# Optimization experiments

Measured on AMD Instinct MI355X. Metric: run time of the kernel, lower is better.

## Reference

```python
import jax, jax.numpy as jnp
import numpy as np
import math

INPUT_SIZE = 1024
HIDDEN_SIZE = 1024
BATCH = 4096


def setup_inputs() -> dict:
    key = jax.random.key(0)
    ks = jax.random.split(key, 16)
    stddev = 1.0 / math.sqrt(HIDDEN_SIZE)

    def unif(k, shape):
        return jax.random.uniform(k, shape, minval=-stddev, maxval=stddev, dtype=jnp.float32)

    inp = {
        'x': jax.random.normal(ks[0], (BATCH, INPUT_SIZE), dtype=jnp.float32),
        'h_prev': jax.random.normal(ks[1], (BATCH, HIDDEN_SIZE), dtype=jnp.float32),
        'c_prev': jax.random.normal(ks[2], (BATCH, HIDDEN_SIZE), dtype=jnp.float32),
        'igx': unif(ks[3], (INPUT_SIZE, HIDDEN_SIZE)),
        'igu': unif(ks[4], (HIDDEN_SIZE, HIDDEN_SIZE)),
        'ib': unif(ks[5], (HIDDEN_SIZE,)),
        'fgx': unif(ks[6], (INPUT_SIZE, HIDDEN_SIZE)),
        'fgu': unif(ks[7], (HIDDEN_SIZE, HIDDEN_SIZE)),
        'fb': unif(ks[8], (HIDDEN_SIZE,)),
        'ogx': unif(ks[9], (INPUT_SIZE, HIDDEN_SIZE)),
        'ogu': unif(ks[10], (HIDDEN_SIZE, HIDDEN_SIZE)),
        'ob': unif(ks[11], (HIDDEN_SIZE,)),
        'cgx': unif(ks[12], (INPUT_SIZE, HIDDEN_SIZE)),
        'cgu': unif(ks[13], (HIDDEN_SIZE, HIDDEN_SIZE)),
        'cb': unif(ks[14], (HIDDEN_SIZE,)),
    }
    return inp


def reference(x, h_prev, c_prev, igx, igu, ib, fgx, fgu, fb, ogx, ogu, ob, cgx, cgu, cb):
    # Fuse the 8 gate matmuls into 2 GEMMs via concatenated weights.
    # Wx: [input_size, 4H], Wh: [hidden, 4H], b: [4H]; gate order i,f,o,c.
    Wx = jnp.concatenate([igx, fgx, ogx, cgx], axis=1)
    Wh = jnp.concatenate([igu, fgu, ogu, cgu], axis=1)
    b = jnp.concatenate([ib, fb, ob, cb], axis=0)
    gates = x @ Wx + h_prev @ Wh + b  # [B, 4H]
    H = c_prev.shape[-1]
    ig = jax.nn.sigmoid(gates[:, 0 * H:1 * H])
    fg = jax.nn.sigmoid(gates[:, 1 * H:2 * H])
    og = jax.nn.sigmoid(gates[:, 2 * H:3 * H])
    cc = jnp.tanh(gates[:, 3 * H:4 * H])
    c = fg * c_prev + ig * cc
    h = og * jnp.tanh(c)
    return (h, c)
```

## Files before the change

### kernel.cpp

```cpp
#include <hip/hip_runtime.h>
#include <hip/hip_bf16.h>

typedef unsigned short u16;
typedef unsigned int u32;
typedef short bf16x8 __attribute__((ext_vector_type(8)));
typedef float f32x4 __attribute__((ext_vector_type(4)));
typedef u16 u16x8 __attribute__((ext_vector_type(8)));

#define HID 1024
#define BATCH 4096
#define KTOT 2048
#define NT 32
#define LDS_OP 16384

__device__ __forceinline__ u16 f2bf(float f) {
  u32 v = __builtin_bit_cast(u32, f);
  u32 r = (v + 0x7fffu + ((v >> 16) & 1u)) >> 16;
  return (u16)r;
}
__device__ __forceinline__ float sigmoid_fast(float x) {
  return 1.0f / (1.0f + __expf(-x));
}
__device__ __forceinline__ float tanh_fast(float x) {
  return 2.0f * sigmoid_fast(2.0f * x) - 1.0f;
}
__device__ __forceinline__ void gl_lds16(const void* g, void* l) {
  __builtin_amdgcn_global_load_lds(
      (const __attribute__((address_space(1))) u32*)g,
      (__attribute__((address_space(3))) u32*)l, 16, 0, 0);
}

__global__ __launch_bounds__(256) void prep_all(
    const float* __restrict__ x, const float* __restrict__ hp,
    const float* __restrict__ igx, const float* __restrict__ fgx,
    const float* __restrict__ ogx, const float* __restrict__ cgx,
    const float* __restrict__ igu, const float* __restrict__ fgu,
    const float* __restrict__ ogu, const float* __restrict__ cgu,
    u16* __restrict__ xh, u16* __restrict__ bt) {
  __shared__ u16 lds[64 * 66];
  if (blockIdx.x < 4096) {
    int c = blockIdx.x * 256 + threadIdx.x;
    int row = c >> 8;
    int col0 = (c & 255) << 3;
    const float* src = (col0 < 1024)
                           ? (x + (size_t)row * 1024 + col0)
                           : (hp + (size_t)row * 1024 + (col0 - 1024));
    f32x4 a = *(const f32x4*)(src);
    f32x4 b = *(const f32x4*)(src + 4);
    u16x8 v;
#pragma unroll
    for (int j = 0; j < 4; ++j) { v[j] = f2bf(a[j]); v[j + 4] = f2bf(b[j]); }
    *(u16x8*)(xh + (size_t)row * KTOT + col0) = v;
    return;
  }
  const float* srcs[8] = {igx, fgx, ogx, cgx, igu, fgu, ogu, cgu};
  int bid = blockIdx.x - 4096;
  int m = bid >> 8;
  int tile = bid & 255;
  int th = tile & 15, tk = tile >> 4;
  int h0 = th << 6, k0 = tk << 6;
  int g = m & 3, which = m >> 2;
  const float* W = srcs[m] + (size_t)k0 * HID + h0;

  int t = threadIdx.x;
  int r1 = t >> 4;
  int c1 = (t & 15) << 2;
#pragma unroll
  for (int p = 0; p < 4; ++p) {
    int row = (p << 4) + r1;
    f32x4 v = *(const f32x4*)(W + (size_t)row * HID + c1);
    u32 p0 = (u32)f2bf(v[0]) | ((u32)f2bf(v[1]) << 16);
    u32 p1 = (u32)f2bf(v[2]) | ((u32)f2bf(v[3]) << 16);
    u32* d = (u32*)&lds[row * 66 + c1];
    d[0] = p0;
    d[1] = p1;
  }
  __syncthreads();
  int nl = t >> 2;
  int kc = t & 3;
  int row_np = ((h0 >> 4) << 6) + ((nl >> 4) << 6) + (g << 4) + (nl & 15);
  size_t dst = (size_t)row_np * KTOT + (size_t)which * 1024 + k0;
  u16x8 a2, b2;
#pragma unroll
  for (int j = 0; j < 8; ++j) {
    a2[j] = lds[(kc * 8 + j) * 66 + nl];
    b2[j] = lds[(kc * 8 + 32 + j) * 66 + nl];
  }
  *(u16x8*)(&bt[dst + kc * 8]) = a2;
  *(u16x8*)(&bt[dst + kc * 8 + 32]) = b2;
}

__device__ __forceinline__ void stage(int s, const u16* aS, const u16* bS,
                                      u16* lds, int sx) {
  if (s >= 4 * NT) return;
  int ts = s >> 2, hh = s & 3;
  int op = (hh >> 1) ^ 1;
  int rb = (hh & 1) << 7;
  const u16* src = (op ? bS : aS) + (size_t)rb * KTOT + ts * 64;
  u16* dst = lds + ((((ts & 1) << 1) + op) * LDS_OP) + (rb << 6) + sx * 8;
  gl_lds16(src, dst);
  gl_lds16(src + (size_t)64 * KTOT, dst + 4096);
}

__global__ __launch_bounds__(512, 2) void lstm_gemm(
    const u16* __restrict__ xh, const u16* __restrict__ bt,
    const float* __restrict__ cprev,
    const float* __restrict__ ib, const float* __restrict__ fb,
    const float* __restrict__ ob, const float* __restrict__ cb,
    float* __restrict__ hout, float* __restrict__ cout) {
  __shared__ __align__(16) u16 lds[2 * 2 * LDS_OP];

  int sx = threadIdx.x;
  int bid = blockIdx.x;
  int xcd = bid & 7, lid = bid >> 3;
  int brow = ((xcd & 3) << 2) | (lid & 3);
  int bcol = ((xcd >> 2) << 3) | (lid >> 2);

  int w = sx >> 6, l = sx & 63;
  int wr = (w >> 2) << 7;
  int wc = (w & 3) << 6;
  int lrow = l & 15, q = l >> 4;
  int grow = brow << 8;

  int prow = sx >> 3;
  int koff = ((sx & 7) ^ (prow & 7)) << 3;
  const u16* aSrc = xh + (size_t)(grow + prow) * KTOT + koff;
  const u16* bSrc = bt + (size_t)(bcol * 256 + prow) * KTOT + koff;

  int aoff = (wr + lrow) << 6;
  int boff = (wc + lrow) << 6;
  int pc0 = (q ^ (lrow & 7)) << 3;
  int pc1 = ((q + 4) ^ (lrow & 7)) << 3;

  f32x4 acc[8][4] = {};
  bf16x8 af[2][2], bfr[4][2];

  stage(0, aSrc, bSrc, lds, sx);
  stage(1, aSrc, bSrc, lds, sx);
  stage(2, aSrc, bSrc, lds, sx);
  stage(3, aSrc, bSrc, lds, sx);
  stage(4, aSrc, bSrc, lds, sx);
  asm volatile("s_waitcnt vmcnt(2)");
  __builtin_amdgcn_s_barrier();
  __builtin_amdgcn_sched_barrier(0);

#define RDA(i, s) (*(const bf16x8*)(Ab + aoff + (i) * 1024 + ((s) ? pc1 : pc0)))
#define RDB(j, s) (*(const bf16x8*)(Bb + boff + (j) * 1024 + ((s) ? pc1 : pc0)))

#define DO_PHASE(K_, SS_)                                                     \
  {                                                                           \
    af[0][0] = RDA(2 * (K_), 0);                                              \
    af[0][1] = RDA(2 * (K_), 1);                                              \
    af[1][0] = RDA(2 * (K_) + 1, 0);                                          \
    af[1][1] = RDA(2 * (K_) + 1, 1);                                          \
    if ((K_) == 0) {                                                          \
      bfr[0][0] = RDB(0, 0); bfr[0][1] = RDB(0, 1);                           \
      bfr[1][0] = RDB(1, 0); bfr[1][1] = RDB(1, 1);                           \
      bfr[2][0] = RDB(2, 0); bfr[2][1] = RDB(2, 1);                           \
      bfr[3][0] = RDB(3, 0); bfr[3][1] = RDB(3, 1);                           \
    }                                                                         \
    stage(SS_, aSrc, bSrc, lds, sx);                                          \
    __builtin_amdgcn_s_barrier();                                             \
    asm volatile("s_waitcnt lgkmcnt(0)");                                     \
    __builtin_amdgcn_sched_barrier(0);                                        \
    __builtin_amdgcn_s_setprio(1);                                            \
    _Pragma("unroll") for (int s2 = 0; s2 < 2; ++s2) {                        \
      _Pragma("unroll") for (int j = 0; j < 4; ++j) {                         \
        acc[2 * (K_)][j] = __builtin_amdgcn_mfma_f32_16x16x32_bf16(           \
            af[0][s2], bfr[j][s2], acc[2 * (K_)][j], 0, 0, 0);                \
        acc[2 * (K_) + 1][j] = __builtin_amdgcn_mfma_f32_16x16x32_bf16(       \
            af[1][s2], bfr[j][s2], acc[2 * (K_) + 1][j], 0, 0, 0);            \
      }                                                                       \
    }                                                                         \
    __builtin_amdgcn_s_setprio(0);                                            \
    __builtin_amdgcn_sched_barrier(0);                                        \
  }

#pragma unroll 2
  for (int t = 0; t < NT; ++t) {
    const u16* Ab = lds + ((t & 1) << 1) * LDS_OP;
    const u16* Bb = Ab + LDS_OP;
    int s0 = 4 * t + 5;
    DO_PHASE(0, s0)
    __builtin_amdgcn_s_barrier();
    DO_PHASE(1, s0 + 1)
    __builtin_amdgcn_s_barrier();
    DO_PHASE(2, s0 + 2)
    __builtin_amdgcn_s_barrier();
    DO_PHASE(3, s0 + 3)
    if (t < NT - 2) {
      asm volatile("s_waitcnt vmcnt(2)");
      __builtin_amdgcn_sched_barrier(0);
    } else {
      asm volatile("s_waitcnt vmcnt(0)");
      __builtin_amdgcn_sched_barrier(0);
    }
    __builtin_amdgcn_s_barrier();
  }
#undef DO_PHASE
#undef RDA
#undef RDB

  int sb = (bcol << 2) + (w & 3);
  int hcol = (sb << 4) + lrow;
  float bi = ib[hcol];
  float bff = fb[hcol];
  float bo = ob[hcol];
  float bc = cb[hcol];

#pragma unroll
  for (int i = 0; i < 8; ++i) {
    int row0 = grow + wr + i * 16 + q * 4;
#pragma unroll
    for (int r = 0; r < 4; ++r) {
      size_t idx = (size_t)(row0 + r) * HID + hcol;
      float gi = sigmoid_fast(acc[i][0][r] + bi);
      float gf = sigmoid_fast(acc[i][1][r] + bff);
      float go = sigmoid_fast(acc[i][2][r] + bo);
      float gc = tanh_fast(acc[i][3][r] + bc);
      float cp = cprev[idx];
      float cv = gf * cp + gi * gc;
      hout[idx] = go * tanh_fast(cv);
      cout[idx] = cv;
    }
  }
}

extern "C" void kernel_launch(void* const* d_in, const int* in_sizes, int n_in,
                              void* d_out, int out_size, void* d_ws, size_t ws_size,
                              hipStream_t stream) {
  const float* x   = (const float*)d_in[0];
  const float* hp  = (const float*)d_in[1];
  const float* cp  = (const float*)d_in[2];
  const float* igx = (const float*)d_in[3];
  const float* igu = (const float*)d_in[4];
  const float* ib  = (const float*)d_in[5];
  const float* fgx = (const float*)d_in[6];
  const float* fgu = (const float*)d_in[7];
  const float* fb  = (const float*)d_in[8];
  const float* ogx = (const float*)d_in[9];
  const float* ogu = (const float*)d_in[10];
  const float* ob  = (const float*)d_in[11];
  const float* cgx = (const float*)d_in[12];
  const float* cgu = (const float*)d_in[13];
  const float* cb  = (const float*)d_in[14];

  u16* bt = (u16*)d_ws;
  u16* xh = bt + (size_t)4096 * 2048;
  float* hout = (float*)d_out;
  float* cout = hout + (size_t)BATCH * HID;

  prep_all<<<6144, 256, 0, stream>>>(x, hp, igx, fgx, ogx, cgx,
                                     igu, fgu, ogu, cgu, xh, bt);
  lstm_gemm<<<256, 512, 0, stream>>>(xh, bt, cp, ib, fb, ob, cb,
                                     hout, cout);
}
```

Baseline: 204.4 us.

## Prefetch B tiles two steps ahead with constant LDS offsets and unrolled pipeline

The software pipeline is rebuilt so the B operand for tile t+2 goes into the same LDS buffer right after its fragments are read into registers in phase 0. The A operand for tile t+1 goes into the alternate buffer. The loop is manually unrolled by two with a peeled tail, so all LDS offsets are compile-time constants and the runtime stage() index arithmetic and branches disappear. The intent is a deeper lead for B loads and cheaper address generation. It relies on the vmcnt counts and barriers being exactly right for the new issue order.

```diff
diff --git a/kernel.cpp b/kernel.cpp
--- a/kernel.cpp
+++ b/kernel.cpp
@@ -11,7 +11,10 @@
 #define BATCH 4096
 #define KTOT 2048
 #define NT 32
-#define LDS_OP 16384
+#define A0B 0
+#define B0B 16384
+#define A1B 32768
+#define B1B 49152
 
 __device__ __forceinline__ u16 f2bf(float f) {
   u32 v = __builtin_bit_cast(u32, f);
@@ -90,25 +93,13 @@
   *(u16x8*)(&bt[dst + kc * 8 + 32]) = b2;
 }
 
-__device__ __forceinline__ void stage(int s, const u16* aS, const u16* bS,
-                                      u16* lds, int sx) {
-  if (s >= 4 * NT) return;
-  int ts = s >> 2, hh = s & 3;
-  int op = (hh >> 1) ^ 1;
-  int rb = (hh & 1) << 7;
-  const u16* src = (op ? bS : aS) + (size_t)rb * KTOT + ts * 64;
-  u16* dst = lds + ((((ts & 1) << 1) + op) * LDS_OP) + (rb << 6) + sx * 8;
-  gl_lds16(src, dst);
-  gl_lds16(src + (size_t)64 * KTOT, dst + 4096);
-}
-
 __global__ __launch_bounds__(512, 2) void lstm_gemm(
     const u16* __restrict__ xh, const u16* __restrict__ bt,
     const float* __restrict__ cprev,
     const float* __restrict__ ib, const float* __restrict__ fb,
     const float* __restrict__ ob, const float* __restrict__ cb,
     float* __restrict__ hout, float* __restrict__ cout) {
-  __shared__ __align__(16) u16 lds[2 * 2 * LDS_OP];
+  __shared__ __align__(16) u16 lds[4 * 16384];
 
   int sx = threadIdx.x;
   int bid = blockIdx.x;
@@ -124,8 +115,11 @@
 
   int prow = sx >> 3;
   int koff = ((sx & 7) ^ (prow & 7)) << 3;
-  const u16* aSrc = xh + (size_t)(grow + prow) * KTOT + koff;
-  const u16* bSrc = bt + (size_t)(bcol * 256 + prow) * KTOT + koff;
+  const u16* aS0 = xh + (size_t)(grow + prow) * KTOT + koff;
+  const u16* aS1 = aS0 + (size_t)128 * KTOT;
+  const u16* bS0 = bt + (size_t)(bcol * 256 + prow) * KTOT + koff;
+  const u16* bS1 = bS0 + (size_t)128 * KTOT;
+  int sx8 = sx * 8;
 
   int aoff = (wr + lrow) << 6;
   int boff = (wc + lrow) << 6;
@@ -135,31 +129,36 @@
   f32x4 acc[8][4] = {};
   bf16x8 af[2][2], bfr[4][2];
 
-  stage(0, aSrc, bSrc, lds, sx);
-  stage(1, aSrc, bSrc, lds, sx);
-  stage(2, aSrc, bSrc, lds, sx);
-  stage(3, aSrc, bSrc, lds, sx);
-  stage(4, aSrc, bSrc, lds, sx);
-  asm volatile("s_waitcnt vmcnt(2)");
+#define STG(P_, K_, D_)                                                       \
+  gl_lds16((P_) + (K_), &lds[(D_) + sx8]);                                    \
+  gl_lds16((P_) + (size_t)64 * KTOT + (K_), &lds[(D_) + 4096 + sx8]);
+
+  STG(bS0, 0, B0B)
+  STG(bS1, 0, B0B + 8192)
+  STG(aS0, 0, A0B)
+  STG(aS1, 0, A0B + 8192)
+  STG(bS0, 64, B1B)
+  STG(bS1, 64, B1B + 8192)
+  asm volatile("s_waitcnt vmcnt(4)");
   __builtin_amdgcn_s_barrier();
   __builtin_amdgcn_sched_barrier(0);
 
-#define RDA(i, s) (*(const bf16x8*)(Ab + aoff + (i) * 1024 + ((s) ? pc1 : pc0)))
-#define RDB(j, s) (*(const bf16x8*)(Bb + boff + (j) * 1024 + ((s) ? pc1 : pc0)))
-
-#define DO_PHASE(K_, SS_)                                                     \
+#define RDA(AB_, i, pc) (*(const bf16x8*)&lds[(AB_) + aoff + (i) * 1024 + (pc)])
+#define RDB(BB_, j, pc) (*(const bf16x8*)&lds[(BB_) + boff + (j) * 1024 + (pc)])
+
+#define DO_PHASE(K_, AB_, BB_, STG_STMT_)                                     \
   {                                                                           \
-    af[0][0] = RDA(2 * (K_), 0);                                              \
-    af[0][1] = RDA(2 * (K_), 1);                                              \
-    af[1][0] = RDA(2 * (K_) + 1, 0);                                          \
-    af[1][1] = RDA(2 * (K_) + 1, 1);                                          \
+    af[0][0] = RDA(AB_, 2 * (K_), pc0);                                       \
+    af[0][1] = RDA(AB_, 2 * (K_), pc1);                                       \
+    af[1][0] = RDA(AB_, 2 * (K_) + 1, pc0);                                   \
+    af[1][1] = RDA(AB_, 2 * (K_) + 1, pc1);                                   \
     if ((K_) == 0) {                                                          \
-      bfr[0][0] = RDB(0, 0); bfr[0][1] = RDB(0, 1);                           \
-      bfr[1][0] = RDB(1, 0); bfr[1][1] = RDB(1, 1);                           \
-      bfr[2][0] = RDB(2, 0); bfr[2][1] = RDB(2, 1);                           \
-      bfr[3][0] = RDB(3, 0); bfr[3][1] = RDB(3, 1);                           \
+      bfr[0][0] = RDB(BB_, 0, pc0); bfr[0][1] = RDB(BB_, 0, pc1);             \
+      bfr[1][0] = RDB(BB_, 1, pc0); bfr[1][1] = RDB(BB_, 1, pc1);             \
+      bfr[2][0] = RDB(BB_, 2, pc0); bfr[2][1] = RDB(BB_, 2, pc1);             \
+      bfr[3][0] = RDB(BB_, 3, pc0); bfr[3][1] = RDB(BB_, 3, pc1);             \
     }                                                                         \
-    stage(SS_, aSrc, bSrc, lds, sx);                                          \
+    STG_STMT_                                                                 \
     __builtin_amdgcn_s_barrier();                                             \
     asm volatile("s_waitcnt lgkmcnt(0)");                                     \
     __builtin_amdgcn_sched_barrier(0);                                        \
@@ -176,30 +175,60 @@
     __builtin_amdgcn_sched_barrier(0);                                        \
   }
 
-#pragma unroll 2
-  for (int t = 0; t < NT; ++t) {
-    const u16* Ab = lds + ((t & 1) << 1) * LDS_OP;
-    const u16* Bb = Ab + LDS_OP;
-    int s0 = 4 * t + 5;
-    DO_PHASE(0, s0)
-    __builtin_amdgcn_s_barrier();
-    DO_PHASE(1, s0 + 1)
-    __builtin_amdgcn_s_barrier();
-    DO_PHASE(2, s0 + 2)
-    __builtin_amdgcn_s_barrier();
-    DO_PHASE(3, s0 + 3)
-    if (t < NT - 2) {
-      asm volatile("s_waitcnt vmcnt(2)");
-      __builtin_amdgcn_sched_barrier(0);
-    } else {
-      asm volatile("s_waitcnt vmcnt(0)");
-      __builtin_amdgcn_sched_barrier(0);
-    }
-    __builtin_amdgcn_s_barrier();
+#define BAR() __builtin_amdgcn_s_barrier();
+#define BOUND(N_)                                                             \
+  asm volatile("s_waitcnt vmcnt(" #N_ ")");                                   \
+  __builtin_amdgcn_sched_barrier(0);                                          \
+  __builtin_amdgcn_s_barrier();
+
+  for (int tp = 0; tp < 15; ++tp) {
+    int t = 2 * tp;
+    int kA = (t + 1) << 6;
+    int kB = (t + 2) << 6;
+    int kA2 = kB;
+    int kB2 = (t + 3) << 6;
+    DO_PHASE(0, A0B, B0B, STG(aS0, kA, A1B))
+    BAR()
+    DO_PHASE(1, A0B, B0B, STG(aS1, kA, A1B + 8192))
+    BAR()
+    DO_PHASE(2, A0B, B0B, STG(bS0, kB, B0B))
+    BAR()
+    DO_PHASE(3, A0B, B0B, STG(bS1, kB, B0B + 8192))
+    BOUND(4)
+    DO_PHASE(0, A1B, B1B, STG(aS0, kA2, A0B))
+    BAR()
+    DO_PHASE(1, A1B, B1B, STG(aS1, kA2, A0B + 8192))
+    BAR()
+    DO_PHASE(2, A1B, B1B, STG(bS0, kB2, B1B))
+    BAR()
+    DO_PHASE(3, A1B, B1B, STG(bS1, kB2, B1B + 8192))
+    BOUND(4)
+  }
+
+  {
+    const int kA = 31 << 6;
+    DO_PHASE(0, A0B, B0B, STG(aS0, kA, A1B))
+    BAR()
+    DO_PHASE(1, A0B, B0B, STG(aS1, kA, A1B + 8192))
+    BAR()
+    DO_PHASE(2, A0B, B0B, )
+    BAR()
+    DO_PHASE(3, A0B, B0B, )
+    BOUND(0)
+    DO_PHASE(0, A1B, B1B, )
+    BAR()
+    DO_PHASE(1, A1B, B1B, )
+    BAR()
+    DO_PHASE(2, A1B, B1B, )
+    BAR()
+    DO_PHASE(3, A1B, B1B, )
   }
 #undef DO_PHASE
 #undef RDA
 #undef RDB
+#undef STG
+#undef BAR
+#undef BOUND
 
   int sb = (bcol << 2) + (w & 3);
   int hcol = (sb << 4) + lrow;
```

After: 205.9 us. About the same (+0.7%).
